# Optimization experiments

Hardware: AMD Instinct MI355X
Metric: run time of the kernel (lower is better)

Reference implementation:

```python
import jax, jax.numpy as jnp
import numpy as np

IN_DIMS = (8, 16, 8)
EMBED = 1024
HEADS = 16
HEAD_DIM = EMBED // HEADS
RANK = 16
CORE_SHAPES = [(1, 8, 8, RANK), (RANK, 16, 16, RANK), (RANK, 8, 8, 1)]


def tt_linear(x, cores, bias):
    """Apply a TT-matrix to x: [N, prod(IN_DIMS)] -> [N, prod(out_dims)].

    Cores G_k: [r_{k-1}, i_k, o_k, r_k], r_0 = r_d = 1. Sequential chain of
    small rank-bounded contractions, faithful to TTLinear.forward.
    """
    N = x.shape[0]
    t = x.reshape(N, 1, 1, -1)  # (N, O_done, r, I_rest)
    for G, i in zip(cores, IN_DIMS):
        rest = t.shape[-1] // i
        t = t.reshape(N, t.shape[1], t.shape[2], i, rest)
        # contract input mode i and left rank r -> output mode q and right rank s
        t = jnp.einsum('norik,riqs->noqsk', t, G)
        t = t.reshape(N, t.shape[1] * t.shape[2], t.shape[3], -1)
    return t.reshape(N, -1) + bias


def setup_inputs() -> dict:
    key = jax.random.key(0)
    ks = iter(jax.random.split(key, 32))
    inp = {"query": jax.random.normal(next(ks), (2, 2048, EMBED), dtype=jnp.float32)}
    for name in ("wq", "wk", "wv", "wo"):
        for ci, shp in enumerate(CORE_SHAPES):
            inp[f"{name}_c{ci}"] = jax.random.normal(next(ks), shp, dtype=jnp.float32) * 0.3
        inp[f"{name}_b"] = jax.random.normal(next(ks), (EMBED,), dtype=jnp.float32) * 0.02
    return inp


def reference(query, wq_c0, wq_c1, wq_c2, wq_b, wk_c0, wk_c1, wk_c2, wk_b,
              wv_c0, wv_c1, wv_c2, wv_b, wo_c0, wo_c1, wo_c2, wo_b):
    B, Lq, _ = query.shape
    flat = query.reshape(-1, EMBED)
    # self-attention: key = value = query
    Q = tt_linear(flat, (wq_c0, wq_c1, wq_c2), wq_b).reshape(B, Lq, HEADS, HEAD_DIM)
    K = tt_linear(flat, (wk_c0, wk_c1, wk_c2), wk_b).reshape(B, Lq, HEADS, HEAD_DIM)
    V = tt_linear(flat, (wv_c0, wv_c1, wv_c2), wv_b).reshape(B, Lq, HEADS, HEAD_DIM)
    Q = Q.transpose(0, 2, 1, 3)  # bhqd
    K = K.transpose(0, 2, 1, 3)
    V = V.transpose(0, 2, 1, 3)
    scale = HEAD_DIM ** -0.5
    scores = jnp.einsum('bhqd,bhkd->bhqk', Q, K) * scale
    attn = jax.nn.softmax(scores, axis=-1)
    ctx = jnp.einsum('bhqk,bhkd->bhqd', attn, V)
    ctx = ctx.transpose(0, 2, 1, 3).reshape(B * Lq, EMBED)
    out = tt_linear(ctx, (wo_c0, wo_c1, wo_c2), wo_b)
    return out.reshape(B, Lq, EMBED)
```

## Files before the change

kernel.cpp:

```cpp
#include <hip/hip_runtime.h>
#include <hip/hip_bf16.h>
#include <stdint.h>

#define LQ 2048
#define NTOK 4096

typedef __attribute__((ext_vector_type(8))) short short8;
typedef __attribute__((ext_vector_type(4))) float f32x4;
typedef __attribute__((ext_vector_type(16))) float f32x16;
typedef __attribute__((ext_vector_type(4))) unsigned short u16x4;

#define MFMA16(a, b, c) __builtin_amdgcn_mfma_f32_16x16x32_bf16((a), (b), (c), 0, 0, 0)
#define MFMA32(a, b, c) __builtin_amdgcn_mfma_f32_32x32x16_bf16((a), (b), (c), 0, 0, 0)

__device__ __forceinline__ unsigned short f2bf(float x) {
    union { __hip_bfloat16 b; unsigned short u; } v;
    v.b = __float2bfloat16(x);
    return v.u;
}
__device__ __forceinline__ float bf2f(unsigned short h) {
    union { uint32_t u; float f; } v; v.u = ((uint32_t)h) << 16; return v.f;
}
__device__ __forceinline__ unsigned int cvtpk_bf16(float lo, float hi_) {
    unsigned int r;
    asm("v_cvt_pk_bf16_f32 %0, %1, %2" : "=v"(r) : "v"(lo), "v"(hi_));
    return r;
}
__device__ __forceinline__ void permswap(unsigned int &a, unsigned int &b) {
    asm("v_permlane32_swap_b32 %0, %1" : "+v"(a), "+v"(b));
}
__device__ __forceinline__ float fast_exp2(float x) {
    float r;
    asm("v_exp_f32 %0, %1" : "=v"(r) : "v"(x));
    return r;
}

struct CorePtrs {
    const float* c0[4];
    const float* c1[4];
    const float* c2[4];
};

struct QkvOut {
    unsigned short* qhi;
    unsigned short* qlo;
    unsigned short* khi;
    unsigned short* klo;
    unsigned short* vt;
    const float* bias[3];
    float qscale;
};

__global__ __launch_bounds__(256) void prep_kernel(
    CorePtrs cp, unsigned short* __restrict__ Whi, unsigned short* __restrict__ Wlo,
    const float* __restrict__ X, unsigned short* __restrict__ Xhi,
    unsigned short* __restrict__ Xlo)
{
    const int blk = blockIdx.x;
    const int t = threadIdx.x;
    if (blk >= 256) {
        const int i = (blk - 256) * 256 + t;
        const float4 v = ((const float4*)X)[i];
        u16x4 hi, lo;
        float vv[4] = {v.x, v.y, v.z, v.w};
#pragma unroll
        for (int j = 0; j < 4; ++j) {
            unsigned short h = f2bf(vv[j]);
            hi[j] = h;
            lo[j] = f2bf(vv[j] - bf2f(h));
        }
        ((u16x4*)Xhi)[i] = hi;
        ((u16x4*)Xlo)[i] = lo;
        return;
    }
    __shared__ float B1[16 * 16 * 16];
    const int p  = blk >> 6;
    const int i0 = (blk & 63) >> 3;
    const int q0 = blk & 7;
    const float* __restrict__ c0 = cp.c0[p];
    const float* __restrict__ c1 = cp.c1[p];
    const float* __restrict__ c2 = cp.c2[p];

    float g0[16];
#pragma unroll
    for (int s = 0; s < 16; ++s) g0[s] = c0[(i0 * 8 + q0) * 16 + s];

    for (int idx = t; idx < 4096; idx += 256) {
        const int s2 = idx & 15;
        const int q1 = (idx >> 4) & 15;
        const int i1 = idx >> 8;
        float acc = 0.f;
#pragma unroll
        for (int s = 0; s < 16; ++s)
            acc += g0[s] * c1[((s * 16 + i1) * 16 + q1) * 16 + s2];
        B1[idx] = acc;
    }
    __syncthreads();

    const size_t base = (size_t)p * 1024 * 1024;
    for (int idx = t; idx < 16384; idx += 256) {
        const int q2 = idx & 7;
        const int i2 = (idx >> 3) & 7;
        const int q1 = (idx >> 6) & 15;
        const int i1 = idx >> 10;
        float acc = 0.f;
#pragma unroll
        for (int s2 = 0; s2 < 16; ++s2)
            acc += B1[(i1 * 16 + q1) * 16 + s2] * c2[(s2 * 8 + i2) * 8 + q2];
        const int o = q0 * 128 + q1 * 8 + q2;
        const int e = i0 * 128 + i1 * 8 + i2;
        const unsigned short hi = f2bf(acc);
        Whi[base + o * 1024 + e] = hi;
        Wlo[base + o * 1024 + e] = f2bf(acc - bf2f(hi));
    }
}

__global__ __launch_bounds__(256) void gemm_qkv_kernel(
    const unsigned short* __restrict__ Xh, const unsigned short* __restrict__ Xl,
    const unsigned short* __restrict__ Wh, const unsigned short* __restrict__ Wl,
    QkvOut op)
{
    __shared__ unsigned short Ah[128 * 32];
    __shared__ unsigned short Bh[128 * 32];
    __shared__ unsigned short Al[128 * 32];
    __shared__ unsigned short Bl[128 * 32];

    const int t = threadIdx.x;
    const int l = t & 63;
    const int w = t >> 6;
    const int wr = (w >> 1) * 64, wc = (w & 1) * 64;
    const int bm = blockIdx.y * 128, bn = blockIdx.x * 128;
    const bool is_v = (bn >> 10) == 2;

    f32x4 acc[4][4];
#pragma unroll
    for (int i = 0; i < 4; ++i)
#pragma unroll
        for (int j = 0; j < 4; ++j) acc[i][j] = (f32x4){0.f, 0.f, 0.f, 0.f};

    const int srow = t >> 1;
    const int sch  = (t & 1) * 2;
    const int ssel = (srow >> 1) & 3;
    const int sd0  = srow * 32 + (((sch)     ^ ssel) << 3);
    const int sd1  = srow * 32 + (((sch + 1) ^ ssel) << 3);
    const size_t xoff = (size_t)(bm + srow) * 1024 + sch * 8;
    const size_t woff = (size_t)(bn + srow) * 1024 + sch * 8;

    const int fsel = ((l & 15) >> 1) & 3;
    const int fpos = ((l >> 4) ^ fsel) << 3;
    const int fra  = (wr + (l & 15)) * 32 + fpos;
    const int frb  = (wc + (l & 15)) * 32 + fpos;

    short8 pXh0, pXh1, pWh0, pWh1, pXl0, pXl1, pWl0, pWl1;
    pXh0 = *(const short8*)&Xh[xoff];     pXh1 = *(const short8*)&Xh[xoff + 8];
    pWh0 = *(const short8*)&Wh[woff];     pWh1 = *(const short8*)&Wh[woff + 8];
    if (!is_v) {
        pXl0 = *(const short8*)&Xl[xoff]; pXl1 = *(const short8*)&Xl[xoff + 8];
        pWl0 = *(const short8*)&Wl[woff]; pWl1 = *(const short8*)&Wl[woff + 8];
    }

    for (int e0 = 0; e0 < 1024; e0 += 32) {
        __syncthreads();
        *(short8*)&Ah[sd0] = pXh0; *(short8*)&Ah[sd1] = pXh1;
        *(short8*)&Bh[sd0] = pWh0; *(short8*)&Bh[sd1] = pWh1;
        if (!is_v) {
            *(short8*)&Al[sd0] = pXl0; *(short8*)&Al[sd1] = pXl1;
            *(short8*)&Bl[sd0] = pWl0; *(short8*)&Bl[sd1] = pWl1;
        }
        __syncthreads();

        if (e0 + 32 < 1024) {
            const size_t xo = xoff + e0 + 32, wo = woff + e0 + 32;
            pXh0 = *(const short8*)&Xh[xo];     pXh1 = *(const short8*)&Xh[xo + 8];
            pWh0 = *(const short8*)&Wh[wo];     pWh1 = *(const short8*)&Wh[wo + 8];
            if (!is_v) {
                pXl0 = *(const short8*)&Xl[xo]; pXl1 = *(const short8*)&Xl[xo + 8];
                pWl0 = *(const short8*)&Wl[wo]; pWl1 = *(const short8*)&Wl[wo + 8];
            }
        }

        short8 af[4], bfv[4], afl[4], bfl[4];
#pragma unroll
        for (int rb = 0; rb < 4; ++rb) {
            af[rb]  = *(const short8*)&Ah[fra + rb * 512];
            bfv[rb] = *(const short8*)&Bh[frb + rb * 512];
        }
#pragma unroll
        for (int rb = 0; rb < 4; ++rb)
#pragma unroll
            for (int cb = 0; cb < 4; ++cb)
                acc[rb][cb] = MFMA16(af[rb], bfv[cb], acc[rb][cb]);
        if (!is_v) {
#pragma unroll
            for (int rb = 0; rb < 4; ++rb) afl[rb] = *(const short8*)&Al[fra + rb * 512];
#pragma unroll
            for (int rb = 0; rb < 4; ++rb)
#pragma unroll
                for (int cb = 0; cb < 4; ++cb)
                    acc[rb][cb] = MFMA16(afl[rb], bfv[cb], acc[rb][cb]);
#pragma unroll
            for (int rb = 0; rb < 4; ++rb) bfl[rb] = *(const short8*)&Bl[frb + rb * 512];
#pragma unroll
            for (int rb = 0; rb < 4; ++rb)
#pragma unroll
                for (int cb = 0; cb < 4; ++cb)
                    acc[rb][cb] = MFMA16(af[rb], bfl[cb], acc[rb][cb]);
        }
    }

    const int p = bn >> 10;
    const float* __restrict__ bp = op.bias[p];
    const int bnl = bn & 1023;
    const int r0 = (l >> 4) * 4;
    const int cc = l & 15;

    if (p < 2) {
        unsigned short* __restrict__ yh = (p == 0) ? op.qhi : op.khi;
        unsigned short* __restrict__ yl = (p == 0) ? op.qlo : op.klo;
        const float osc = (p == 0) ? op.qscale : 1.0f;
#pragma unroll
        for (int rb = 0; rb < 4; ++rb)
#pragma unroll
            for (int cb = 0; cb < 4; ++cb) {
                const int col = bnl + wc + cb * 16 + cc;
                const float bv = bp[col];
#pragma unroll
                for (int r = 0; r < 4; ++r) {
                    const int row = bm + wr + rb * 16 + r0 + r;
                    const float v = (acc[rb][cb][r] + bv) * osc;
                    const unsigned short hi = f2bf(v);
                    yh[(size_t)row * 1024 + col] = hi;
                    yl[(size_t)row * 1024 + col] = f2bf(v - bf2f(hi));
                }
            }
    } else {
        unsigned short* __restrict__ vt = op.vt;
#pragma unroll
        for (int rb = 0; rb < 4; ++rb)
#pragma unroll
            for (int cb = 0; cb < 4; ++cb) {
                const int col = bnl + wc + cb * 16 + cc;
                const float bv = bp[col];
                u16x4 pk;
#pragma unroll
                for (int r = 0; r < 4; ++r)
                    pk[r] = f2bf(acc[rb][cb][r] + bv);
                const int row0 = bm + wr + rb * 16 + r0;
                *(u16x4*)&vt[(size_t)col * 4096 + row0] = pk;
            }
    }
}

__global__ __launch_bounds__(256) void gemm_out_kernel(
    const unsigned short* __restrict__ Xh,
    const unsigned short* __restrict__ Wh,
    const float* __restrict__ bias,
    float* __restrict__ Yf)
{
    __shared__ unsigned short Ah[64 * 32];
    __shared__ unsigned short Bh[128 * 32];

    const int t = threadIdx.x;
    const int l = t & 63;
    const int w = t >> 6;
    const int wr = (w >> 1) * 32, wc = (w & 1) * 64;
    const int bm = blockIdx.y * 64, bn = blockIdx.x * 128;

    f32x4 acc[2][4];
#pragma unroll
    for (int i = 0; i < 2; ++i)
#pragma unroll
        for (int j = 0; j < 4; ++j) acc[i][j] = (f32x4){0.f, 0.f, 0.f, 0.f};

    const int arow = t >> 2, ach = t & 3;
    const int asd  = arow * 32 + ((ach ^ ((arow >> 1) & 3)) << 3);
    const size_t xoff = (size_t)(bm + arow) * 1024 + ach * 8;
    const int brow = t >> 1, bch = (t & 1) * 2;
    const int bsel = (brow >> 1) & 3;
    const int bsd0 = brow * 32 + (((bch)     ^ bsel) << 3);
    const int bsd1 = brow * 32 + (((bch + 1) ^ bsel) << 3);
    const size_t woff = (size_t)(bn + brow) * 1024 + bch * 8;

    const int fsel = ((l & 15) >> 1) & 3;
    const int fpos = ((l >> 4) ^ fsel) << 3;
    const int fra  = (wr + (l & 15)) * 32 + fpos;
    const int frb  = (wc + (l & 15)) * 32 + fpos;

    short8 pA0, pB0, pB1;
    pA0 = *(const short8*)&Xh[xoff];
    pB0 = *(const short8*)&Wh[woff]; pB1 = *(const short8*)&Wh[woff + 8];

    for (int e0 = 0; e0 < 1024; e0 += 32) {
        __syncthreads();
        *(short8*)&Ah[asd]  = pA0;
        *(short8*)&Bh[bsd0] = pB0; *(short8*)&Bh[bsd1] = pB1;
        __syncthreads();

        if (e0 + 32 < 1024) {
            pA0 = *(const short8*)&Xh[xoff + e0 + 32];
            pB0 = *(const short8*)&Wh[woff + e0 + 32];
            pB1 = *(const short8*)&Wh[woff + e0 + 40];
        }

        short8 af[2], bfv[4];
#pragma unroll
        for (int rb = 0; rb < 2; ++rb) af[rb] = *(const short8*)&Ah[fra + rb * 512];
#pragma unroll
        for (int cb = 0; cb < 4; ++cb) bfv[cb] = *(const short8*)&Bh[frb + cb * 512];
#pragma unroll
        for (int rb = 0; rb < 2; ++rb)
#pragma unroll
            for (int cb = 0; cb < 4; ++cb)
                acc[rb][cb] = MFMA16(af[rb], bfv[cb], acc[rb][cb]);
    }

    const int r0 = (l >> 4) * 4;
    const int cc = l & 15;
#pragma unroll
    for (int rb = 0; rb < 2; ++rb)
#pragma unroll
        for (int cb = 0; cb < 4; ++cb) {
            const int col = bn + wc + cb * 16 + cc;
            const float bv = bias[col];
#pragma unroll
            for (int r = 0; r < 4; ++r) {
                const int row = bm + wr + rb * 16 + r0 + r;
                Yf[(size_t)row * 1024 + col] = acc[rb][cb][r] + bv;
            }
        }
}

__global__ __launch_bounds__(256) void attn_kernel(
    const unsigned short* __restrict__ Qh, const unsigned short* __restrict__ Ql,
    const unsigned short* __restrict__ Kh_g, const unsigned short* __restrict__ Kl_g,
    const unsigned short* __restrict__ VT, unsigned short* __restrict__ CTX)
{
    __shared__ unsigned short Khs[2][64 * 64];
    __shared__ unsigned short Kls[2][64 * 64];
    __shared__ unsigned short Vts[2][64 * 64];

    const int t = threadIdx.x;
    const int l = t & 63;
    const int w = t >> 6;
    const int qt = blockIdx.x, h = blockIdx.y, b = blockIdx.z;
    const int lq = l & 31;
    const int hi = l >> 5;
    const int tokq = b * LQ + qt * 128 + w * 32;

    short8 qhf[4], qlf[4];
    {
        const size_t qr = (size_t)(tokq + lq) * 1024 + h * 64 + hi * 8;
#pragma unroll
        for (int ds = 0; ds < 4; ++ds) {
            qhf[ds] = *(const short8*)&Qh[qr + ds * 16];
            qlf[ds] = *(const short8*)&Ql[qr + ds * 16];
        }
    }

    f32x16 o0, o1;
#pragma unroll
    for (int i = 0; i < 16; ++i) { o0[i] = 0.f; o1[i] = 0.f; }
    float m = -1e30f, lsum = 0.f;

    const int srow = t >> 2;
    const int sch  = (t & 3) * 2;
    int sdst[2];
#pragma unroll
    for (int it = 0; it < 2; ++it)
        sdst[it] = srow * 64 + (((sch + it) ^ (srow & 7)) << 3);

    const unsigned short* pkh = Kh_g + (size_t)(b * LQ + srow) * 1024 + h * 64 + sch * 8;
    const unsigned short* pkl = Kl_g + (size_t)(b * LQ + srow) * 1024 + h * 64 + sch * 8;
    const unsigned short* pvt = VT + (size_t)(h * 64 + srow) * 4096 + b * LQ + sch * 8;

    short8 pf_kh[2], pf_kl[2], pf_vt[2];
    pf_kh[0] = *(const short8*)pkh;       pf_kh[1] = *(const short8*)(pkh + 8);
    pf_kl[0] = *(const short8*)pkl;       pf_kl[1] = *(const short8*)(pkl + 8);
    pf_vt[0] = *(const short8*)pvt;       pf_vt[1] = *(const short8*)(pvt + 8);

    const int lq7 = lq & 7;
    int qkoff[4], pvslot[4];
#pragma unroll
    for (int i = 0; i < 4; ++i) {
        qkoff[i]  = lq * 64 + (((2 * i + hi) ^ lq7) << 3);
        pvslot[i] = (((2 * i + hi) ^ lq7) << 3);
    }

    int cur = 0;
    for (int kt = 0; kt < 32; ++kt) {
#pragma unroll
        for (int it = 0; it < 2; ++it) {
            *(short8*)&Khs[cur][sdst[it]] = pf_kh[it];
            *(short8*)&Kls[cur][sdst[it]] = pf_kl[it];
            *(short8*)&Vts[cur][sdst[it]] = pf_vt[it];
        }
        if (kt < 31) {
            pkh += 64 * 1024; pkl += 64 * 1024; pvt += 64;
            pf_kh[0] = *(const short8*)pkh;  pf_kh[1] = *(const short8*)(pkh + 8);
            pf_kl[0] = *(const short8*)pkl;  pf_kl[1] = *(const short8*)(pkl + 8);
            pf_vt[0] = *(const short8*)pvt;  pf_vt[1] = *(const short8*)(pvt + 8);
        }
        __syncthreads();

        f32x16 s0, s1;
#pragma unroll
        for (int i = 0; i < 16; ++i) { s0[i] = 0.f; s1[i] = 0.f; }
        __builtin_amdgcn_s_setprio(1);
#pragma unroll
        for (int ds = 0; ds < 4; ++ds) {
            const int off = qkoff[ds];
            short8 kh0 = *(const short8*)&Khs[cur][off];
            short8 kh1 = *(const short8*)&Khs[cur][off + 2048];
            short8 kl0 = *(const short8*)&Kls[cur][off];
            short8 kl1 = *(const short8*)&Kls[cur][off + 2048];
            s0 = MFMA32(kh0, qhf[ds], s0);
            s1 = MFMA32(kh1, qhf[ds], s1);
            s0 = MFMA32(kl0, qhf[ds], s0);
            s1 = MFMA32(kl1, qhf[ds], s1);
            s0 = MFMA32(kh0, qlf[ds], s0);
            s1 = MFMA32(kh1, qlf[ds], s1);
        }
        __builtin_amdgcn_s_setprio(0);

        float v0 = fmaxf(s0[0], s0[1]), v1 = fmaxf(s0[2], s0[3]);
        float v2 = fmaxf(s0[4], s0[5]), v3 = fmaxf(s0[6], s0[7]);
#pragma unroll
        for (int i = 8; i < 16; i += 4) {
            v0 = fmaxf(v0, fmaxf(s0[i], s0[i + 1]));
            v1 = fmaxf(v1, fmaxf(s0[i + 2], s0[i + 3]));
        }
#pragma unroll
        for (int i = 0; i < 16; i += 4) {
            v2 = fmaxf(v2, fmaxf(s1[i], s1[i + 1]));
            v3 = fmaxf(v3, fmaxf(s1[i + 2], s1[i + 3]));
        }
        float vm = fmaxf(fmaxf(v0, v1), fmaxf(v2, v3));
        vm = fmaxf(vm, __shfl_xor(vm, 32));
        const float mg = fmaxf(m, vm);
        if (__any(mg > m + 8.f)) {
            const float mu = (mg > m + 8.f) ? mg : m;
            const float alpha = fast_exp2(m - mu);
            lsum *= alpha;
            o0 *= alpha;
            o1 *= alpha;
            m = mu;
        }
        float p0 = 0.f, p1 = 0.f, p2 = 0.f, p3 = 0.f;
#pragma unroll
        for (int i = 0; i < 16; i += 4) {
            s0[i]     = fast_exp2(s0[i] - m);     p0 += s0[i];
            s0[i + 1] = fast_exp2(s0[i + 1] - m); p1 += s0[i + 1];
            s0[i + 2] = fast_exp2(s0[i + 2] - m); p2 += s0[i + 2];
            s0[i + 3] = fast_exp2(s0[i + 3] - m); p3 += s0[i + 3];
        }
#pragma unroll
        for (int i = 0; i < 16; i += 4) {
            s1[i]     = fast_exp2(s1[i] - m);     p0 += s1[i];
            s1[i + 1] = fast_exp2(s1[i + 1] - m); p1 += s1[i + 1];
            s1[i + 2] = fast_exp2(s1[i + 2] - m); p2 += s1[i + 2];
            s1[i + 3] = fast_exp2(s1[i + 3] - m); p3 += s1[i + 3];
        }
        lsum += (p0 + p1) + (p2 + p3);

        unsigned int pw[4][4];
        {
            unsigned int a, bb;
            a = cvtpk_bf16(s0[0], s0[1]); bb = cvtpk_bf16(s0[4], s0[5]);
            permswap(a, bb); pw[0][0] = a; pw[0][2] = bb;
            a = cvtpk_bf16(s0[2], s0[3]); bb = cvtpk_bf16(s0[6], s0[7]);
            permswap(a, bb); pw[0][1] = a; pw[0][3] = bb;
            a = cvtpk_bf16(s0[8], s0[9]); bb = cvtpk_bf16(s0[12], s0[13]);
            permswap(a, bb); pw[1][0] = a; pw[1][2] = bb;
            a = cvtpk_bf16(s0[10], s0[11]); bb = cvtpk_bf16(s0[14], s0[15]);
            permswap(a, bb); pw[1][1] = a; pw[1][3] = bb;
            a = cvtpk_bf16(s1[0], s1[1]); bb = cvtpk_bf16(s1[4], s1[5]);
            permswap(a, bb); pw[2][0] = a; pw[2][2] = bb;
            a = cvtpk_bf16(s1[2], s1[3]); bb = cvtpk_bf16(s1[6], s1[7]);
            permswap(a, bb); pw[2][1] = a; pw[2][3] = bb;
            a = cvtpk_bf16(s1[8], s1[9]); bb = cvtpk_bf16(s1[12], s1[13]);
            permswap(a, bb); pw[3][0] = a; pw[3][2] = bb;
            a = cvtpk_bf16(s1[10], s1[11]); bb = cvtpk_bf16(s1[14], s1[15]);
            permswap(a, bb); pw[3][1] = a; pw[3][3] = bb;
        }

        __builtin_amdgcn_s_setprio(1);
#pragma unroll
        for (int ks = 0; ks < 4; ++ks) {
            union { unsigned int u[4]; short8 v; } pa;
            pa.u[0] = pw[ks][0]; pa.u[1] = pw[ks][1];
            pa.u[2] = pw[ks][2]; pa.u[3] = pw[ks][3];
            const int slot = pvslot[ks];
            short8 va = *(const short8*)&Vts[cur][lq * 64 + slot];
            short8 vb = *(const short8*)&Vts[cur][(32 + lq) * 64 + slot];
            o0 = MFMA32(va, pa.v, o0);
            o1 = MFMA32(vb, pa.v, o1);
        }
        __builtin_amdgcn_s_setprio(0);
        cur ^= 1;
    }

    lsum += __shfl_xor(lsum, 32);
    const float inv = 1.f / lsum;
    const size_t orow = (size_t)(tokq + lq) * 1024 + h * 64 + hi * 4;
#pragma unroll
    for (int g = 0; g < 4; ++g) {
        u16x4 pack0, pack1;
#pragma unroll
        for (int j = 0; j < 4; ++j) {
            pack0[j] = f2bf(o0[4 * g + j] * inv);
            pack1[j] = f2bf(o1[4 * g + j] * inv);
        }
        *(u16x4*)&CTX[orow + 8 * g]      = pack0;
        *(u16x4*)&CTX[orow + 32 + 8 * g] = pack1;
    }
}

extern "C" void kernel_launch(void* const* d_in, const int* in_sizes, int n_in,
                              void* d_out, int out_size, void* d_ws, size_t ws_size,
                              hipStream_t stream)
{
    (void)in_sizes; (void)n_in; (void)out_size; (void)ws_size;
    const float* query = (const float*)d_in[0];
    char* base = (char*)d_ws;
    const size_t MB = 1 << 20;
    unsigned short* Whi = (unsigned short*)(base + 0 * MB);
    unsigned short* Wlo = (unsigned short*)(base + 8 * MB);
    unsigned short* Xhi = (unsigned short*)(base + 16 * MB);
    unsigned short* Xlo = (unsigned short*)(base + 24 * MB);
    unsigned short* Qhi = (unsigned short*)(base + 32 * MB);
    unsigned short* Qlo = (unsigned short*)(base + 40 * MB);
    unsigned short* Khi = (unsigned short*)(base + 48 * MB);
    unsigned short* Klo = (unsigned short*)(base + 56 * MB);
    unsigned short* VTp = (unsigned short*)(base + 72 * MB);
    unsigned short* CTX = (unsigned short*)(base + 16 * MB);

    CorePtrs cp;
    for (int p = 0; p < 4; ++p) {
        cp.c0[p] = (const float*)d_in[1 + 4 * p];
        cp.c1[p] = (const float*)d_in[2 + 4 * p];
        cp.c2[p] = (const float*)d_in[3 + 4 * p];
    }
    const size_t WSZ = (size_t)1024 * 1024;
    const float QSCALE = 0.125f * 1.44269504088896340736f;

    prep_kernel<<<4352, 256, 0, stream>>>(cp, Whi, Wlo, query, Xhi, Xlo);

    QkvOut op;
    op.qhi = Qhi; op.qlo = Qlo; op.khi = Khi; op.klo = Klo; op.vt = VTp;
    op.bias[0] = (const float*)d_in[4];
    op.bias[1] = (const float*)d_in[8];
    op.bias[2] = (const float*)d_in[12];
    op.qscale = QSCALE;
    gemm_qkv_kernel<<<dim3(24, 32), 256, 0, stream>>>(Xhi, Xlo, Whi, Wlo, op);

    attn_kernel<<<dim3(16, 16, 2), 256, 0, stream>>>(Qhi, Qlo, Khi, Klo, VTp, CTX);

    gemm_out_kernel<<<dim3(8, 64), 256, 0, stream>>>(
        CTX, Whi + 3 * WSZ, (const float*)d_in[16], (float*)d_out);
}
```

Measured before the change: 275.1 us.

## Shrink output GEMM tile to 64x64 and simplify softmax max/sum chains

The output-projection GEMM moves from 64x128 to 64x64 block tiles, doubling the grid to 1024 blocks so more CUs are busy, at the cost of reloading activations more often. Separately, the attention softmax swaps the multi-accumulator max and exp-sum reductions for single-accumulator chains. This shortens the instruction sequence but lengthens the dependency chain. The two changes are unrelated.

```diff
diff --git a/kernel.cpp b/kernel.cpp
--- a/kernel.cpp
+++ b/kernel.cpp
@@ -258,59 +258,54 @@
     float* __restrict__ Yf)
 {
     __shared__ unsigned short Ah[64 * 32];
-    __shared__ unsigned short Bh[128 * 32];
+    __shared__ unsigned short Bh[64 * 32];
 
     const int t = threadIdx.x;
     const int l = t & 63;
     const int w = t >> 6;
-    const int wr = (w >> 1) * 32, wc = (w & 1) * 64;
-    const int bm = blockIdx.y * 64, bn = blockIdx.x * 128;
-
-    f32x4 acc[2][4];
+    const int wr = (w >> 1) * 32, wc = (w & 1) * 32;
+    const int bm = blockIdx.y * 64, bn = blockIdx.x * 64;
+
+    f32x4 acc[2][2];
 #pragma unroll
     for (int i = 0; i < 2; ++i)
 #pragma unroll
-        for (int j = 0; j < 4; ++j) acc[i][j] = (f32x4){0.f, 0.f, 0.f, 0.f};
-
-    const int arow = t >> 2, ach = t & 3;
-    const int asd  = arow * 32 + ((ach ^ ((arow >> 1) & 3)) << 3);
-    const size_t xoff = (size_t)(bm + arow) * 1024 + ach * 8;
-    const int brow = t >> 1, bch = (t & 1) * 2;
-    const int bsel = (brow >> 1) & 3;
-    const int bsd0 = brow * 32 + (((bch)     ^ bsel) << 3);
-    const int bsd1 = brow * 32 + (((bch + 1) ^ bsel) << 3);
-    const size_t woff = (size_t)(bn + brow) * 1024 + bch * 8;
+        for (int j = 0; j < 2; ++j) acc[i][j] = (f32x4){0.f, 0.f, 0.f, 0.f};
+
+    const int srow = t >> 2, sch = t & 3;
+    const int sd   = srow * 32 + ((sch ^ ((srow >> 1) & 3)) << 3);
+    const size_t xoff = (size_t)(bm + srow) * 1024 + sch * 8;
+    const size_t woff = (size_t)(bn + srow) * 1024 + sch * 8;
 
     const int fsel = ((l & 15) >> 1) & 3;
     const int fpos = ((l >> 4) ^ fsel) << 3;
     const int fra  = (wr + (l & 15)) * 32 + fpos;
     const int frb  = (wc + (l & 15)) * 32 + fpos;
 
-    short8 pA0, pB0, pB1;
-    pA0 = *(const short8*)&Xh[xoff];
-    pB0 = *(const short8*)&Wh[woff]; pB1 = *(const short8*)&Wh[woff + 8];
+    short8 pA, pB;
+    pA = *(const short8*)&Xh[xoff];
+    pB = *(const short8*)&Wh[woff];
 
     for (int e0 = 0; e0 < 1024; e0 += 32) {
         __syncthreads();
-        *(short8*)&Ah[asd]  = pA0;
-        *(short8*)&Bh[bsd0] = pB0; *(short8*)&Bh[bsd1] = pB1;
+        *(short8*)&Ah[sd] = pA;
+        *(short8*)&Bh[sd] = pB;
         __syncthreads();
 
         if (e0 + 32 < 1024) {
-            pA0 = *(const short8*)&Xh[xoff + e0 + 32];
-            pB0 = *(const short8*)&Wh[woff + e0 + 32];
-            pB1 = *(const short8*)&Wh[woff + e0 + 40];
-        }
-
-        short8 af[2], bfv[4];
+            pA = *(const short8*)&Xh[xoff + e0 + 32];
+            pB = *(const short8*)&Wh[woff + e0 + 32];
+        }
+
+        short8 af[2], bfv[2];
 #pragma unroll
         for (int rb = 0; rb < 2; ++rb) af[rb] = *(const short8*)&Ah[fra + rb * 512];
 #pragma unroll
-        for (int cb = 0; cb < 4; ++cb) bfv[cb] = *(const short8*)&Bh[frb + cb * 512];
+        for (int cb = 0; cb < 2; ++cb) bfv[cb] = *(const short8*)&Bh[frb + cb * 512];
 #pragma unroll
         for (int rb = 0; rb < 2; ++rb)
 #pragma unroll
-            for (int cb = 0; cb < 4; ++cb)
+            for (int cb = 0; cb < 2; ++cb)
                 acc[rb][cb] = MFMA16(af[rb], bfv[cb], acc[rb][cb]);
     }
 
@@ -319,7 +314,7 @@
 #pragma unroll
     for (int rb = 0; rb < 2; ++rb)
 #pragma unroll
-        for (int cb = 0; cb < 4; ++cb) {
+        for (int cb = 0; cb < 2; ++cb) {
             const int col = bn + wc + cb * 16 + cc;
             const float bv = bias[col];
 #pragma unroll
@@ -422,19 +417,13 @@
         }
         __builtin_amdgcn_s_setprio(0);
 
-        float v0 = fmaxf(s0[0], s0[1]), v1 = fmaxf(s0[2], s0[3]);
-        float v2 = fmaxf(s0[4], s0[5]), v3 = fmaxf(s0[6], s0[7]);
-#pragma unroll
-        for (int i = 8; i < 16; i += 4) {
-            v0 = fmaxf(v0, fmaxf(s0[i], s0[i + 1]));
-            v1 = fmaxf(v1, fmaxf(s0[i + 2], s0[i + 3]));
-        }
-#pragma unroll
-        for (int i = 0; i < 16; i += 4) {
-            v2 = fmaxf(v2, fmaxf(s1[i], s1[i + 1]));
-            v3 = fmaxf(v3, fmaxf(s1[i + 2], s1[i + 3]));
-        }
-        float vm = fmaxf(fmaxf(v0, v1), fmaxf(v2, v3));
+        float vm = fmaxf(fmaxf(s0[0], s0[1]), s0[2]);
+#pragma unroll
+        for (int i = 3; i < 15; i += 2) vm = fmaxf(fmaxf(s0[i], s0[i + 1]), vm);
+        vm = fmaxf(fmaxf(s0[15], s1[0]), vm);
+#pragma unroll
+        for (int i = 1; i < 15; i += 2) vm = fmaxf(fmaxf(s1[i], s1[i + 1]), vm);
+        vm = fmaxf(s1[15], vm);
         vm = fmaxf(vm, __shfl_xor(vm, 32));
         const float mg = fmaxf(m, vm);
         if (__any(mg > m + 8.f)) {
@@ -445,22 +434,12 @@
             o1 *= alpha;
             m = mu;
         }
-        float p0 = 0.f, p1 = 0.f, p2 = 0.f, p3 = 0.f;
-#pragma unroll
-        for (int i = 0; i < 16; i += 4) {
-            s0[i]     = fast_exp2(s0[i] - m);     p0 += s0[i];
-            s0[i + 1] = fast_exp2(s0[i + 1] - m); p1 += s0[i + 1];
-            s0[i + 2] = fast_exp2(s0[i + 2] - m); p2 += s0[i + 2];
-            s0[i + 3] = fast_exp2(s0[i + 3] - m); p3 += s0[i + 3];
-        }
-#pragma unroll
-        for (int i = 0; i < 16; i += 4) {
-            s1[i]     = fast_exp2(s1[i] - m);     p0 += s1[i];
-            s1[i + 1] = fast_exp2(s1[i + 1] - m); p1 += s1[i + 1];
-            s1[i + 2] = fast_exp2(s1[i + 2] - m); p2 += s1[i + 2];
-            s1[i + 3] = fast_exp2(s1[i + 3] - m); p3 += s1[i + 3];
-        }
-        lsum += (p0 + p1) + (p2 + p3);
+        float ps = 0.f;
+#pragma unroll
+        for (int i = 0; i < 16; ++i) { s0[i] = fast_exp2(s0[i] - m); ps += s0[i]; }
+#pragma unroll
+        for (int i = 0; i < 16; ++i) { s1[i] = fast_exp2(s1[i] - m); ps += s1[i]; }
+        lsum += ps;
 
         unsigned int pw[4][4];
         {
@@ -555,6 +534,6 @@
 
     attn_kernel<<<dim3(16, 16, 2), 256, 0, stream>>>(Qhi, Qlo, Khi, Klo, VTp, CTX);
 
-    gemm_out_kernel<<<dim3(8, 64), 256, 0, stream>>>(
+    gemm_out_kernel<<<dim3(16, 64), 256, 0, stream>>>(
         CTX, Whi + 3 * WSZ, (const float*)d_in[16], (float*)d_out);
 }
```

New measurement: 269.0 us. 2.2% less time.
